# Kernel optimization log

Hardware: AMD Instinct MI355X
Metric: run time of the kernel (lower is better)

## Reference

```python
import jax, jax.numpy as jnp
import numpy as np

HEAD_SIZE = 64   # baseChn * max_channel_ratio
NUM_HEADS = 2
LEAKY_ALPHA = 0.3  # tf.keras.layers.LeakyReLU default


def setup_inputs() -> dict:
    key = jax.random.key(0)
    ks = jax.random.split(key, 6)
    x = jax.random.normal(ks[0], (96, 48, 512), dtype=jnp.float32)
    y = jax.random.uniform(ks[1], (96, 64, 64), dtype=jnp.float32)
    nItem = jax.random.uniform(ks[2], (96,), dtype=jnp.float32, minval=1.0, maxval=48.0)
    W_proj = jax.random.normal(ks[3], (512, 64), dtype=jnp.float32) * 0.05
    W1 = jax.random.normal(ks[4], (64, 128), dtype=jnp.float32) * 0.1
    W2 = jax.random.normal(ks[5], (2, 1), dtype=jnp.float32)
    return {"x": x, "y": y, "nItem": nItem, "W_proj": W_proj, "W1": W1, "W2": W2}


def reference(x, y, nItem, W_proj, W1, W2):
    # fc_cnn_proj: Dense(64, gelu exact, no bias)
    gallery = jax.nn.gelu(jnp.matmul(x, W_proj), approximate=False)  # [Sx, Nx, 64]
    Sx, Nx, _ = gallery.shape
    Sy, Ny, _ = y.shape
    sqrt_hs = jnp.sqrt(jnp.float32(HEAD_SIZE))
    # shared linear (no bias) then split heads: [S, H, N, hs]
    px = jnp.matmul(gallery, W1).reshape(Sx, Nx, NUM_HEADS, HEAD_SIZE).transpose(0, 2, 1, 3)
    py = jnp.matmul(y, W1).reshape(Sy, Ny, NUM_HEADS, HEAD_SIZE).transpose(0, 2, 1, 3)
    # pairwise cross-set attention maps: [Sy, Sx, H, Ny, Nx]
    att = jnp.einsum('yhmd,xhnd->yxhmn', py, px) / sqrt_hs
    att = jnp.where(att > 0, att, LEAKY_ALPHA * att)
    # reduce over both item axes, normalize by nItem[x] and nItemMax_y
    sc = att.sum(axis=(3, 4)) / nItem[None, :, None] / jnp.float32(Ny)  # [Sy, Sx, H]
    scores = jnp.matmul(sc, W2)  # linear2: Dense(1, no bias) -> [Sy, Sx, 1]
    return scores
```

## Files before the change

kernel.cpp:

```cpp
#include <hip/hip_runtime.h>
#include <hip/hip_bf16.h>


typedef short bf16x8 __attribute__((ext_vector_type(8)));
typedef float f32x4 __attribute__((ext_vector_type(4)));

__device__ __forceinline__ unsigned short f2bf(float v) {
  __hip_bfloat16 b = __float2bfloat16(v);
  return *reinterpret_cast<unsigned short*>(&b);
}

__device__ __forceinline__ bf16x8 load8_cvt(const float* __restrict__ p) {
  f32x4 v0 = *reinterpret_cast<const f32x4*>(p);
  f32x4 v1 = *reinterpret_cast<const f32x4*>(p + 4);
  bf16x8 r;
  r[0] = (short)f2bf(v0[0]); r[1] = (short)f2bf(v0[1]);
  r[2] = (short)f2bf(v0[2]); r[3] = (short)f2bf(v0[3]);
  r[4] = (short)f2bf(v1[0]); r[5] = (short)f2bf(v1[1]);
  r[6] = (short)f2bf(v1[2]); r[7] = (short)f2bf(v1[3]);
  return r;
}

__global__ __launch_bounds__(256) void k_prep(const float* __restrict__ x,
                                              const float* __restrict__ y,
                                              const float* __restrict__ Wp,
                                              const float* __restrict__ W1,
                                              unsigned short* __restrict__ pyf,
                                              unsigned short* __restrict__ pxf) {
  __shared__ unsigned short w1f[8192];
  __shared__ unsigned short wpf[8192];
  __shared__ unsigned short gal[4][1152];
  int t = threadIdx.x;
  int lane = t & 63, w = t >> 6;
  int b = blockIdx.x;

#pragma unroll
  for (int it = 0; it < 32; ++it) {
    int idx = it * 256 + t;
    int k = idx >> 7, d = idx & 127;
    int l = (d & 15) + 16 * ((k >> 3) & 3);
    int f = (k >> 5) * 8 + (d >> 4);
    w1f[f * 512 + l * 8 + (k & 7)] = f2bf(W1[idx]);
  }
  if (b >= 72) {
    __syncthreads();
    int yi = b - 72;
    const bf16x8* WF = reinterpret_cast<const bf16x8*>(w1f);
    int row0 = yi * 64 + w * 16 + (lane & 15);
    const float* yb = y + (size_t)row0 * 64 + 8 * (lane >> 4);
    bf16x8 a0 = load8_cvt(yb);
    bf16x8 a1 = load8_cvt(yb + 32);
    f32x4 acc[8];
#pragma unroll
    for (int nt = 0; nt < 8; ++nt) acc[nt] = (f32x4){0.f, 0.f, 0.f, 0.f};
#pragma unroll
    for (int nt = 0; nt < 8; ++nt) {
      acc[nt] = __builtin_amdgcn_mfma_f32_16x16x32_bf16(a0, WF[nt * 64 + lane], acc[nt], 0, 0, 0);
      acc[nt] = __builtin_amdgcn_mfma_f32_16x16x32_bf16(a1, WF[(8 + nt) * 64 + lane], acc[nt], 0, 0, 0);
    }
    int r_hi = (lane >> 4) * 4;
#pragma unroll
    for (int nt = 0; nt < 8; ++nt) {
      int d = nt * 16 + (lane & 15);
      int h = d >> 6, dd = d & 63;
      int kc = dd >> 5, q = (dd >> 3) & 3, i = dd & 7;
#pragma unroll
      for (int j = 0; j < 4; ++j) {
        int m = w * 16 + r_hi + j;
        int mt = m >> 4, rr = m & 15;
        size_t idx = ((size_t)((yi * 2 + h) * 8 + mt * 2 + kc)) * 512 + (rr + (q << 4)) * 8 + i;
        pyf[idx] = f2bf(acc[nt][j]);
      }
    }
  } else {
    int rowbase = b * 64;
    const bf16x8* WPF = reinterpret_cast<const bf16x8*>(wpf);
    const bf16x8* WF = reinterpret_cast<const bf16x8*>(w1f);
    int rloc = rowbase + w * 16 + (lane & 15);
    const float* xb = x + (size_t)rloc * 512 + 8 * (lane >> 4);
    f32x4 acc1[4];
#pragma unroll
    for (int nt = 0; nt < 4; ++nt) acc1[nt] = (f32x4){0.f, 0.f, 0.f, 0.f};
#pragma unroll
    for (int q = 0; q < 4; ++q) {
      if (q) __syncthreads();
#pragma unroll
      for (int it = 0; it < 32; ++it) {
        int idx = it * 256 + t;
        int kq = idx >> 6, c = idx & 63;
        int l = (c & 15) + 16 * ((kq >> 3) & 3);
        int g = ((kq >> 5) & 3) * 4 + (c >> 4);
        wpf[g * 512 + l * 8 + (kq & 7)] = f2bf(Wp[(q * 128 + kq) * 64 + c]);
      }
      __syncthreads();
#pragma unroll
      for (int kk = 0; kk < 4; ++kk) {
        int kc = q * 4 + kk;
        bf16x8 a = load8_cvt(xb + 32 * kc);
#pragma unroll
        for (int nt = 0; nt < 4; ++nt)
          acc1[nt] = __builtin_amdgcn_mfma_f32_16x16x32_bf16(a, WPF[(kk * 4 + nt) * 64 + lane], acc1[nt], 0, 0, 0);
      }
    }
#pragma unroll
    for (int nt = 0; nt < 4; ++nt)
#pragma unroll
      for (int j = 0; j < 4; ++j) {
        float s = acc1[nt][j];
        float ge = 0.5f * s * (1.0f + erff(s * 0.70710678118654752f));
        int rl = (lane >> 4) * 4 + j;
        int c = nt * 16 + (lane & 15);
        gal[w][rl * 72 + c] = f2bf(ge);
      }
    const unsigned short* gp = &gal[w][(lane & 15) * 72 + 8 * (lane >> 4)];
    bf16x8 g0 = *reinterpret_cast<const bf16x8*>(gp);
    bf16x8 g1 = *reinterpret_cast<const bf16x8*>(gp + 32);
    f32x4 acc2[8];
#pragma unroll
    for (int nt = 0; nt < 8; ++nt) acc2[nt] = (f32x4){0.f, 0.f, 0.f, 0.f};
#pragma unroll
    for (int nt = 0; nt < 8; ++nt) {
      acc2[nt] = __builtin_amdgcn_mfma_f32_16x16x32_bf16(g0, WF[nt * 64 + lane], acc2[nt], 0, 0, 0);
      acc2[nt] = __builtin_amdgcn_mfma_f32_16x16x32_bf16(g1, WF[(8 + nt) * 64 + lane], acc2[nt], 0, 0, 0);
    }
    int r_hi = (lane >> 4) * 4;
#pragma unroll
    for (int nt = 0; nt < 8; ++nt) {
      int d = nt * 16 + (lane & 15);
      int h = d >> 6, dd = d & 63;
      int kc = dd >> 5, q2 = (dd >> 3) & 3, i = dd & 7;
#pragma unroll
      for (int j = 0; j < 4; ++j) {
        int row = rowbase + w * 16 + r_hi + j;
        int xi = row / 48, n = row % 48;
        int nt3 = n >> 4, rr = n & 15;
        size_t idx = ((size_t)((xi * 2 + h) * 6 + nt3 * 2 + kc)) * 512 + (rr + (q2 << 4)) * 8 + i;
        pxf[idx] = f2bf(acc2[nt][j]);
      }
    }
  }
}

__global__ __launch_bounds__(256) void k_att(const unsigned short* __restrict__ pyf_u,
                                             const unsigned short* __restrict__ pxf_u,
                                             const float* __restrict__ nItem,
                                             const float* __restrict__ W2,
                                             float* __restrict__ out) {
  int lane = threadIdx.x & 63;
  int w = threadIdx.x >> 6;
  int bid = blockIdx.x;
  int yb = bid >> 5, xq = bid & 31;
  int yi = yb * 4 + w;
  int xi0 = xq * 3;
  const bf16x8* PA = reinterpret_cast<const bf16x8*>(pyf_u);
  const bf16x8* PB = reinterpret_cast<const bf16x8*>(pxf_u);

  float w2h0 = W2[0], w2h1 = W2[1];
  float nI0 = nItem[xi0], nI1 = nItem[xi0 + 1], nI2 = nItem[xi0 + 2];

  f32x4 zero4 = {0.f, 0.f, 0.f, 0.f};
  asm volatile("" : "+v"(zero4));

  bf16x8 A8[16];
  size_t abase = (size_t)(yi * 2) * 512 + lane;
#pragma unroll
  for (int f = 0; f < 8; ++f) {
    A8[f]     = PA[abase + f * 64];
    A8[8 + f] = PA[abase + 512 + f * 64];
  }

  float c3h0 = 0.3f * w2h0, c7h0 = 0.7f * w2h0;
  float c3h1 = 0.3f * w2h1, c7h1 = 0.7f * w2h1;

  bf16x8 Bc[6], Bn[6];
  size_t bb0 = (size_t)((xi0 * 2 + 0) * 6) * 64 + lane;
#pragma unroll
  for (int f = 0; f < 6; ++f) Bc[f] = PB[bb0 + f * 64];

  f32x4 res4[3];
#pragma unroll
  for (int g = 0; g < 3; ++g) res4[g] = (f32x4){0.f, 0.f, 0.f, 0.f};

#pragma unroll
  for (int s = 0; s < 6; ++s) {
    const int h = s / 3, g = s % 3;
    if (s < 5) {
      const int s2 = s + 1, h2 = s2 / 3, g2 = s2 % 3;
      size_t bb = (size_t)(((xi0 + g2) * 2 + h2) * 6) * 64 + lane;
#pragma unroll
      for (int f = 0; f < 6; ++f) Bn[f] = PB[bb + f * 64];
    }
    const float c3 = h ? c3h1 : c3h0;
    const float c7 = h ? c7h1 : c7h0;
#pragma unroll
    for (int nt = 0; nt < 3; ++nt)
#pragma unroll
      for (int mt = 0; mt < 4; ++mt) {
        f32x4 acc = __builtin_amdgcn_mfma_f32_16x16x32_bf16(A8[h * 8 + mt * 2], Bc[nt * 2], zero4, 0, 0, 0);
        acc = __builtin_amdgcn_mfma_f32_16x16x32_bf16(A8[h * 8 + mt * 2 + 1], Bc[nt * 2 + 1], acc, 0, 0, 0);
        f32x4 mx = {fmaxf(acc[0], 0.f), fmaxf(acc[1], 0.f), fmaxf(acc[2], 0.f), fmaxf(acc[3], 0.f)};
        res4[g] += acc * c3;
        res4[g] += mx * c7;
      }
#pragma unroll
    for (int f = 0; f < 6; ++f) Bc[f] = Bn[f];
  }

  float tot0 = (res4[0][0] + res4[0][1]) + (res4[0][2] + res4[0][3]);
  float tot1 = (res4[1][0] + res4[1][1]) + (res4[1][2] + res4[1][3]);
  float tot2 = (res4[2][0] + res4[2][1]) + (res4[2][2] + res4[2][3]);
#pragma unroll
  for (int off = 32; off >= 1; off >>= 1) {
    tot0 += __shfl_xor(tot0, off, 64);
    tot1 += __shfl_xor(tot1, off, 64);
    tot2 += __shfl_xor(tot2, off, 64);
  }
  if (lane == 0) {
    out[yi * 96 + xi0 + 0] = tot0 / (512.0f * nI0);
    out[yi * 96 + xi0 + 1] = tot1 / (512.0f * nI1);
    out[yi * 96 + xi0 + 2] = tot2 / (512.0f * nI2);
  }
}

extern "C" void kernel_launch(void* const* d_in, const int* in_sizes, int n_in,
                              void* d_out, int out_size, void* d_ws, size_t ws_size,
                              hipStream_t stream) {
  const float* x     = (const float*)d_in[0];
  const float* y     = (const float*)d_in[1];
  const float* nItem = (const float*)d_in[2];
  const float* Wp    = (const float*)d_in[3];
  const float* W1    = (const float*)d_in[4];
  const float* W2    = (const float*)d_in[5];
  float* out = (float*)d_out;

  unsigned short* pyf = (unsigned short*)d_ws;
  unsigned short* pxf = pyf + 786432;

  hipLaunchKernelGGL(k_prep, dim3(168), dim3(256), 0, stream, x, y, Wp, W1, pyf, pxf);
  hipLaunchKernelGGL(k_att, dim3(768), dim3(256), 0, stream, pyf, pxf, nItem, W2, out);
}
```

Before: 35.52 us.

## Fuse prep and attention kernels with a device-wide atomic barrier

Merges the projection kernel and the attention kernel into one persistent launch of 384 blocks. The first 168 blocks compute the projections, then every block waits on a grid-wide barrier built from atomic counters, with one leader block per XCD issuing a release before all blocks proceed. Each block then handles six x-items instead of three, halving the attention grid. This removes a kernel launch boundary and its tail, but adds a memset launch and spin-waiting, and it relies on all 384 blocks being co-resident to avoid deadlock.

```diff
diff --git a/kernel.cpp b/kernel.cpp
--- a/kernel.cpp
+++ b/kernel.cpp
@@ -4,6 +4,12 @@
 
 typedef short bf16x8 __attribute__((ext_vector_type(8)));
 typedef float f32x4 __attribute__((ext_vector_type(4)));
+
+#define NPROD 168u
+#define NBLK  384
+#define F_PRODCNT 0
+#define F_FLUSHCNT 1
+#define F_CLAIM 2
 
 __device__ __forceinline__ unsigned short f2bf(float v) {
   __hip_bfloat16 b = __float2bfloat16(v);
@@ -21,12 +27,16 @@
   return r;
 }
 
-__global__ __launch_bounds__(256) void k_prep(const float* __restrict__ x,
-                                              const float* __restrict__ y,
-                                              const float* __restrict__ Wp,
-                                              const float* __restrict__ W1,
-                                              unsigned short* __restrict__ pyf,
-                                              unsigned short* __restrict__ pxf) {
+__global__ __launch_bounds__(256, 2) void k_fused(const float* __restrict__ x,
+                                                  const float* __restrict__ y,
+                                                  const float* __restrict__ Wp,
+                                                  const float* __restrict__ W1,
+                                                  const float* __restrict__ nItem,
+                                                  const float* __restrict__ W2,
+                                                  unsigned short* __restrict__ pyf,
+                                                  unsigned short* __restrict__ pxf,
+                                                  unsigned int* flags,
+                                                  float* __restrict__ out) {
   __shared__ unsigned short w1f[8192];
   __shared__ unsigned short wpf[8192];
   __shared__ unsigned short gal[4][1152];
@@ -34,191 +44,202 @@
   int lane = t & 63, w = t >> 6;
   int b = blockIdx.x;
 
-#pragma unroll
-  for (int it = 0; it < 32; ++it) {
-    int idx = it * 256 + t;
-    int k = idx >> 7, d = idx & 127;
-    int l = (d & 15) + 16 * ((k >> 3) & 3);
-    int f = (k >> 5) * 8 + (d >> 4);
-    w1f[f * 512 + l * 8 + (k & 7)] = f2bf(W1[idx]);
+  float w2h0 = W2[0], w2h1 = W2[1];
+  int xi0 = (b & 15) * 6;
+  float nI[6];
+#pragma unroll
+  for (int g = 0; g < 6; ++g) nI[g] = nItem[xi0 + g];
+
+  if (b < (int)NPROD) {
+#pragma unroll
+    for (int it = 0; it < 32; ++it) {
+      int idx = it * 256 + t;
+      int k = idx >> 7, d = idx & 127;
+      int l = (d & 15) + 16 * ((k >> 3) & 3);
+      int f = (k >> 5) * 8 + (d >> 4);
+      w1f[f * 512 + l * 8 + (k & 7)] = f2bf(W1[idx]);
+    }
+    if (b >= 72) {
+      __syncthreads();
+      int yi = b - 72;
+      const bf16x8* WF = reinterpret_cast<const bf16x8*>(w1f);
+      int row0 = yi * 64 + w * 16 + (lane & 15);
+      const float* yb = y + (size_t)row0 * 64 + 8 * (lane >> 4);
+      bf16x8 a0 = load8_cvt(yb);
+      bf16x8 a1 = load8_cvt(yb + 32);
+      f32x4 acc[8];
+#pragma unroll
+      for (int nt = 0; nt < 8; ++nt) acc[nt] = (f32x4){0.f, 0.f, 0.f, 0.f};
+#pragma unroll
+      for (int nt = 0; nt < 8; ++nt) {
+        acc[nt] = __builtin_amdgcn_mfma_f32_16x16x32_bf16(a0, WF[nt * 64 + lane], acc[nt], 0, 0, 0);
+        acc[nt] = __builtin_amdgcn_mfma_f32_16x16x32_bf16(a1, WF[(8 + nt) * 64 + lane], acc[nt], 0, 0, 0);
+      }
+      int r_hi = (lane >> 4) * 4;
+#pragma unroll
+      for (int nt = 0; nt < 8; ++nt) {
+        int d = nt * 16 + (lane & 15);
+        int h = d >> 6, dd = d & 63;
+        int kc = dd >> 5, q = (dd >> 3) & 3, i = dd & 7;
+#pragma unroll
+        for (int j = 0; j < 4; ++j) {
+          int m = w * 16 + r_hi + j;
+          int mt = m >> 4, rr = m & 15;
+          size_t idx = ((size_t)((yi * 2 + h) * 8 + mt * 2 + kc)) * 512 + (rr + (q << 4)) * 8 + i;
+          pyf[idx] = f2bf(acc[nt][j]);
+        }
+      }
+    } else {
+      int rowbase = b * 64;
+      const bf16x8* WPF = reinterpret_cast<const bf16x8*>(wpf);
+      const bf16x8* WF = reinterpret_cast<const bf16x8*>(w1f);
+      int rloc = rowbase + w * 16 + (lane & 15);
+      const float* xb = x + (size_t)rloc * 512 + 8 * (lane >> 4);
+      f32x4 acc1[4];
+#pragma unroll
+      for (int nt = 0; nt < 4; ++nt) acc1[nt] = (f32x4){0.f, 0.f, 0.f, 0.f};
+#pragma unroll
+      for (int q = 0; q < 4; ++q) {
+        if (q) __syncthreads();
+#pragma unroll
+        for (int it = 0; it < 32; ++it) {
+          int idx = it * 256 + t;
+          int kq = idx >> 6, c = idx & 63;
+          int l = (c & 15) + 16 * ((kq >> 3) & 3);
+          int g = ((kq >> 5) & 3) * 4 + (c >> 4);
+          wpf[g * 512 + l * 8 + (kq & 7)] = f2bf(Wp[(q * 128 + kq) * 64 + c]);
+        }
+        __syncthreads();
+#pragma unroll
+        for (int kk = 0; kk < 4; ++kk) {
+          int kc = q * 4 + kk;
+          bf16x8 a = load8_cvt(xb + 32 * kc);
+#pragma unroll
+          for (int nt = 0; nt < 4; ++nt)
+            acc1[nt] = __builtin_amdgcn_mfma_f32_16x16x32_bf16(a, WPF[(kk * 4 + nt) * 64 + lane], acc1[nt], 0, 0, 0);
+        }
+      }
+#pragma unroll
+      for (int nt = 0; nt < 4; ++nt)
+#pragma unroll
+        for (int j = 0; j < 4; ++j) {
+          float s = acc1[nt][j];
+          float ge = 0.5f * s * (1.0f + erff(s * 0.70710678118654752f));
+          int rl = (lane >> 4) * 4 + j;
+          int c = nt * 16 + (lane & 15);
+          gal[w][rl * 72 + c] = f2bf(ge);
+        }
+      const unsigned short* gp = &gal[w][(lane & 15) * 72 + 8 * (lane >> 4)];
+      bf16x8 g0 = *reinterpret_cast<const bf16x8*>(gp);
+      bf16x8 g1 = *reinterpret_cast<const bf16x8*>(gp + 32);
+      f32x4 acc2[8];
+#pragma unroll
+      for (int nt = 0; nt < 8; ++nt) acc2[nt] = (f32x4){0.f, 0.f, 0.f, 0.f};
+#pragma unroll
+      for (int nt = 0; nt < 8; ++nt) {
+        acc2[nt] = __builtin_amdgcn_mfma_f32_16x16x32_bf16(g0, WF[nt * 64 + lane], acc2[nt], 0, 0, 0);
+        acc2[nt] = __builtin_amdgcn_mfma_f32_16x16x32_bf16(g1, WF[(8 + nt) * 64 + lane], acc2[nt], 0, 0, 0);
+      }
+      int r_hi = (lane >> 4) * 4;
+#pragma unroll
+      for (int nt = 0; nt < 8; ++nt) {
+        int d = nt * 16 + (lane & 15);
+        int h = d >> 6, dd = d & 63;
+        int kc = dd >> 5, q2 = (dd >> 3) & 3, i = dd & 7;
+#pragma unroll
+        for (int j = 0; j < 4; ++j) {
+          int row = rowbase + w * 16 + r_hi + j;
+          int xi = row / 48, n = row % 48;
+          int nt3 = n >> 4, rr = n & 15;
+          size_t idx = ((size_t)((xi * 2 + h) * 6 + nt3 * 2 + kc)) * 512 + (rr + (q2 << 4)) * 8 + i;
+          pxf[idx] = f2bf(acc2[nt][j]);
+        }
+      }
+    }
   }
-  if (b >= 72) {
-    __syncthreads();
-    int yi = b - 72;
-    const bf16x8* WF = reinterpret_cast<const bf16x8*>(w1f);
-    int row0 = yi * 64 + w * 16 + (lane & 15);
-    const float* yb = y + (size_t)row0 * 64 + 8 * (lane >> 4);
-    bf16x8 a0 = load8_cvt(yb);
-    bf16x8 a1 = load8_cvt(yb + 32);
-    f32x4 acc[8];
-#pragma unroll
-    for (int nt = 0; nt < 8; ++nt) acc[nt] = (f32x4){0.f, 0.f, 0.f, 0.f};
-#pragma unroll
-    for (int nt = 0; nt < 8; ++nt) {
-      acc[nt] = __builtin_amdgcn_mfma_f32_16x16x32_bf16(a0, WF[nt * 64 + lane], acc[nt], 0, 0, 0);
-      acc[nt] = __builtin_amdgcn_mfma_f32_16x16x32_bf16(a1, WF[(8 + nt) * 64 + lane], acc[nt], 0, 0, 0);
-    }
-    int r_hi = (lane >> 4) * 4;
-#pragma unroll
-    for (int nt = 0; nt < 8; ++nt) {
-      int d = nt * 16 + (lane & 15);
-      int h = d >> 6, dd = d & 63;
-      int kc = dd >> 5, q = (dd >> 3) & 3, i = dd & 7;
-#pragma unroll
-      for (int j = 0; j < 4; ++j) {
-        int m = w * 16 + r_hi + j;
-        int mt = m >> 4, rr = m & 15;
-        size_t idx = ((size_t)((yi * 2 + h) * 8 + mt * 2 + kc)) * 512 + (rr + (q << 4)) * 8 + i;
-        pyf[idx] = f2bf(acc[nt][j]);
-      }
-    }
-  } else {
-    int rowbase = b * 64;
-    const bf16x8* WPF = reinterpret_cast<const bf16x8*>(wpf);
-    const bf16x8* WF = reinterpret_cast<const bf16x8*>(w1f);
-    int rloc = rowbase + w * 16 + (lane & 15);
-    const float* xb = x + (size_t)rloc * 512 + 8 * (lane >> 4);
-    f32x4 acc1[4];
-#pragma unroll
-    for (int nt = 0; nt < 4; ++nt) acc1[nt] = (f32x4){0.f, 0.f, 0.f, 0.f};
-#pragma unroll
-    for (int q = 0; q < 4; ++q) {
-      if (q) __syncthreads();
-#pragma unroll
-      for (int it = 0; it < 32; ++it) {
-        int idx = it * 256 + t;
-        int kq = idx >> 6, c = idx & 63;
-        int l = (c & 15) + 16 * ((kq >> 3) & 3);
-        int g = ((kq >> 5) & 3) * 4 + (c >> 4);
-        wpf[g * 512 + l * 8 + (kq & 7)] = f2bf(Wp[(q * 128 + kq) * 64 + c]);
-      }
-      __syncthreads();
-#pragma unroll
-      for (int kk = 0; kk < 4; ++kk) {
-        int kc = q * 4 + kk;
-        bf16x8 a = load8_cvt(xb + 32 * kc);
-#pragma unroll
-        for (int nt = 0; nt < 4; ++nt)
-          acc1[nt] = __builtin_amdgcn_mfma_f32_16x16x32_bf16(a, WPF[(kk * 4 + nt) * 64 + lane], acc1[nt], 0, 0, 0);
-      }
-    }
-#pragma unroll
-    for (int nt = 0; nt < 4; ++nt)
-#pragma unroll
-      for (int j = 0; j < 4; ++j) {
-        float s = acc1[nt][j];
-        float ge = 0.5f * s * (1.0f + erff(s * 0.70710678118654752f));
-        int rl = (lane >> 4) * 4 + j;
-        int c = nt * 16 + (lane & 15);
-        gal[w][rl * 72 + c] = f2bf(ge);
-      }
-    const unsigned short* gp = &gal[w][(lane & 15) * 72 + 8 * (lane >> 4)];
-    bf16x8 g0 = *reinterpret_cast<const bf16x8*>(gp);
-    bf16x8 g1 = *reinterpret_cast<const bf16x8*>(gp + 32);
-    f32x4 acc2[8];
-#pragma unroll
-    for (int nt = 0; nt < 8; ++nt) acc2[nt] = (f32x4){0.f, 0.f, 0.f, 0.f};
-#pragma unroll
-    for (int nt = 0; nt < 8; ++nt) {
-      acc2[nt] = __builtin_amdgcn_mfma_f32_16x16x32_bf16(g0, WF[nt * 64 + lane], acc2[nt], 0, 0, 0);
-      acc2[nt] = __builtin_amdgcn_mfma_f32_16x16x32_bf16(g1, WF[(8 + nt) * 64 + lane], acc2[nt], 0, 0, 0);
-    }
-    int r_hi = (lane >> 4) * 4;
-#pragma unroll
-    for (int nt = 0; nt < 8; ++nt) {
-      int d = nt * 16 + (lane & 15);
-      int h = d >> 6, dd = d & 63;
-      int kc = dd >> 5, q2 = (dd >> 3) & 3, i = dd & 7;
-#pragma unroll
-      for (int j = 0; j < 4; ++j) {
-        int row = rowbase + w * 16 + r_hi + j;
-        int xi = row / 48, n = row % 48;
-        int nt3 = n >> 4, rr = n & 15;
-        size_t idx = ((size_t)((xi * 2 + h) * 6 + nt3 * 2 + kc)) * 512 + (rr + (q2 << 4)) * 8 + i;
-        pxf[idx] = f2bf(acc2[nt][j]);
-      }
-    }
+
+  __syncthreads();
+  if (t == 0) {
+    if (b < (int)NPROD)
+      __hip_atomic_fetch_add(&flags[F_PRODCNT], 1u, __ATOMIC_RELAXED, __HIP_MEMORY_SCOPE_AGENT);
+    unsigned xcd;
+    asm volatile("s_getreg_b32 %0, hwreg(HW_REG_XCC_ID)" : "=s"(xcd));
+    xcd &= 7u;
+    if (__hip_atomic_fetch_add(&flags[F_CLAIM + xcd], 1u, __ATOMIC_RELAXED, __HIP_MEMORY_SCOPE_AGENT) == 0u) {
+      while (__hip_atomic_load(&flags[F_PRODCNT], __ATOMIC_RELAXED, __HIP_MEMORY_SCOPE_AGENT) != NPROD)
+        __builtin_amdgcn_s_sleep(4);
+      __hip_atomic_fetch_add(&flags[F_FLUSHCNT], 1u, __ATOMIC_RELEASE, __HIP_MEMORY_SCOPE_AGENT);
+    }
+    while (__hip_atomic_load(&flags[F_FLUSHCNT], __ATOMIC_RELAXED, __HIP_MEMORY_SCOPE_AGENT) != 8u)
+      __builtin_amdgcn_s_sleep(4);
   }
-}
-
-__global__ __launch_bounds__(256) void k_att(const unsigned short* __restrict__ pyf_u,
-                                             const unsigned short* __restrict__ pxf_u,
-                                             const float* __restrict__ nItem,
-                                             const float* __restrict__ W2,
-                                             float* __restrict__ out) {
-  int lane = threadIdx.x & 63;
-  int w = threadIdx.x >> 6;
-  int bid = blockIdx.x;
-  int yb = bid >> 5, xq = bid & 31;
-  int yi = yb * 4 + w;
-  int xi0 = xq * 3;
-  const bf16x8* PA = reinterpret_cast<const bf16x8*>(pyf_u);
-  const bf16x8* PB = reinterpret_cast<const bf16x8*>(pxf_u);
-
-  float w2h0 = W2[0], w2h1 = W2[1];
-  float nI0 = nItem[xi0], nI1 = nItem[xi0 + 1], nI2 = nItem[xi0 + 2];
-
-  f32x4 zero4 = {0.f, 0.f, 0.f, 0.f};
-  asm volatile("" : "+v"(zero4));
-
-  bf16x8 A8[16];
-  size_t abase = (size_t)(yi * 2) * 512 + lane;
-#pragma unroll
-  for (int f = 0; f < 8; ++f) {
-    A8[f]     = PA[abase + f * 64];
-    A8[8 + f] = PA[abase + 512 + f * 64];
-  }
-
-  float c3h0 = 0.3f * w2h0, c7h0 = 0.7f * w2h0;
-  float c3h1 = 0.3f * w2h1, c7h1 = 0.7f * w2h1;
-
-  bf16x8 Bc[6], Bn[6];
-  size_t bb0 = (size_t)((xi0 * 2 + 0) * 6) * 64 + lane;
-#pragma unroll
-  for (int f = 0; f < 6; ++f) Bc[f] = PB[bb0 + f * 64];
-
-  f32x4 res4[3];
-#pragma unroll
-  for (int g = 0; g < 3; ++g) res4[g] = (f32x4){0.f, 0.f, 0.f, 0.f};
-
-#pragma unroll
-  for (int s = 0; s < 6; ++s) {
-    const int h = s / 3, g = s % 3;
-    if (s < 5) {
-      const int s2 = s + 1, h2 = s2 / 3, g2 = s2 % 3;
-      size_t bb = (size_t)(((xi0 + g2) * 2 + h2) * 6) * 64 + lane;
-#pragma unroll
-      for (int f = 0; f < 6; ++f) Bn[f] = PB[bb + f * 64];
-    }
-    const float c3 = h ? c3h1 : c3h0;
-    const float c7 = h ? c7h1 : c7h0;
-#pragma unroll
-    for (int nt = 0; nt < 3; ++nt)
-#pragma unroll
-      for (int mt = 0; mt < 4; ++mt) {
-        f32x4 acc = __builtin_amdgcn_mfma_f32_16x16x32_bf16(A8[h * 8 + mt * 2], Bc[nt * 2], zero4, 0, 0, 0);
-        acc = __builtin_amdgcn_mfma_f32_16x16x32_bf16(A8[h * 8 + mt * 2 + 1], Bc[nt * 2 + 1], acc, 0, 0, 0);
-        f32x4 mx = {fmaxf(acc[0], 0.f), fmaxf(acc[1], 0.f), fmaxf(acc[2], 0.f), fmaxf(acc[3], 0.f)};
-        res4[g] += acc * c3;
-        res4[g] += mx * c7;
-      }
-#pragma unroll
-    for (int f = 0; f < 6; ++f) Bc[f] = Bn[f];
-  }
-
-  float tot0 = (res4[0][0] + res4[0][1]) + (res4[0][2] + res4[0][3]);
-  float tot1 = (res4[1][0] + res4[1][1]) + (res4[1][2] + res4[1][3]);
-  float tot2 = (res4[2][0] + res4[2][1]) + (res4[2][2] + res4[2][3]);
-#pragma unroll
-  for (int off = 32; off >= 1; off >>= 1) {
-    tot0 += __shfl_xor(tot0, off, 64);
-    tot1 += __shfl_xor(tot1, off, 64);
-    tot2 += __shfl_xor(tot2, off, 64);
-  }
-  if (lane == 0) {
-    out[yi * 96 + xi0 + 0] = tot0 / (512.0f * nI0);
-    out[yi * 96 + xi0 + 1] = tot1 / (512.0f * nI1);
-    out[yi * 96 + xi0 + 2] = tot2 / (512.0f * nI2);
+  __syncthreads();
+
+  {
+    int yi = (b >> 4) * 4 + w;
+    const bf16x8* PA = reinterpret_cast<const bf16x8*>(pyf);
+    const bf16x8* PB = reinterpret_cast<const bf16x8*>(pxf);
+
+    f32x4 zero4 = {0.f, 0.f, 0.f, 0.f};
+    asm volatile("" : "+v"(zero4));
+
+    bf16x8 A8[16];
+    size_t abase = (size_t)(yi * 2) * 512 + lane;
+#pragma unroll
+    for (int f = 0; f < 8; ++f) {
+      A8[f]     = PA[abase + f * 64];
+      A8[8 + f] = PA[abase + 512 + f * 64];
+    }
+    float c3h0 = 0.3f * w2h0, c7h0 = 0.7f * w2h0;
+    float c3h1 = 0.3f * w2h1, c7h1 = 0.7f * w2h1;
+
+    bf16x8 Bc[6], Bn[6];
+    size_t bb0 = (size_t)((xi0 * 2 + 0) * 6) * 64 + lane;
+#pragma unroll
+    for (int f = 0; f < 6; ++f) Bc[f] = PB[bb0 + f * 64];
+
+    f32x4 res4[6];
+#pragma unroll
+    for (int g = 0; g < 6; ++g) res4[g] = (f32x4){0.f, 0.f, 0.f, 0.f};
+
+#pragma unroll
+    for (int s = 0; s < 12; ++s) {
+      const int h = s & 1, g = s >> 1;
+      if (s < 11) {
+        const int s2 = s + 1, h2 = s2 & 1, g2 = s2 >> 1;
+        size_t bb = (size_t)(((xi0 + g2) * 2 + h2) * 6) * 64 + lane;
+#pragma unroll
+        for (int f = 0; f < 6; ++f) Bn[f] = PB[bb + f * 64];
+      }
+      const float c3 = h ? c3h1 : c3h0;
+      const float c7 = h ? c7h1 : c7h0;
+#pragma unroll
+      for (int nt = 0; nt < 3; ++nt)
+#pragma unroll
+        for (int mt = 0; mt < 4; ++mt) {
+          f32x4 acc = __builtin_amdgcn_mfma_f32_16x16x32_bf16(A8[h * 8 + mt * 2], Bc[nt * 2], zero4, 0, 0, 0);
+          acc = __builtin_amdgcn_mfma_f32_16x16x32_bf16(A8[h * 8 + mt * 2 + 1], Bc[nt * 2 + 1], acc, 0, 0, 0);
+          f32x4 mx = {fmaxf(acc[0], 0.f), fmaxf(acc[1], 0.f), fmaxf(acc[2], 0.f), fmaxf(acc[3], 0.f)};
+          res4[g] += acc * c3;
+          res4[g] += mx * c7;
+        }
+#pragma unroll
+      for (int f = 0; f < 6; ++f) Bc[f] = Bn[f];
+    }
+
+    float tot[6];
+#pragma unroll
+    for (int g = 0; g < 6; ++g)
+      tot[g] = (res4[g][0] + res4[g][1]) + (res4[g][2] + res4[g][3]);
+#pragma unroll
+    for (int off = 32; off >= 1; off >>= 1)
+#pragma unroll
+      for (int g = 0; g < 6; ++g) tot[g] += __shfl_xor(tot[g], off, 64);
+    if (lane == 0) {
+#pragma unroll
+      for (int g = 0; g < 6; ++g)
+        out[yi * 96 + xi0 + g] = tot[g] / (512.0f * nI[g]);
+    }
   }
 }
 
@@ -235,7 +256,9 @@
 
   unsigned short* pyf = (unsigned short*)d_ws;
   unsigned short* pxf = pyf + 786432;
-
-  hipLaunchKernelGGL(k_prep, dim3(168), dim3(256), 0, stream, x, y, Wp, W1, pyf, pxf);
-  hipLaunchKernelGGL(k_att, dim3(768), dim3(256), 0, stream, pyf, pxf, nItem, W2, out);
-}
+  unsigned int* flags = (unsigned int*)(pxf + 589824);
+
+  hipMemsetAsync(flags, 0, 64, stream);
+  hipLaunchKernelGGL(k_fused, dim3(NBLK), dim3(256), 0, stream,
+                     x, y, Wp, W1, nItem, W2, pyf, pxf, flags, out);
+}
```

Result: slower. 55.16 us (+55.3%).

## Pre-swizzle weights to bf16 in a separate kernel and double prep block count

Applied to the files above, without the earlier changes.

A new small kernel converts Wp and W1 to bf16 in MFMA fragment layout once. The prep kernel then copies these layouts into LDS with vector loads instead of having every block convert them element by element. Each prep block now handles 32 rows instead of 64, doubling the grid from 168 to 336 blocks, with the four waves splitting the N tiles. The aim is more parallelism and less redundant weight conversion per block, at the cost of an extra kernel launch and more repeated weight loads in total.

```diff
diff --git a/kernel.cpp b/kernel.cpp
--- a/kernel.cpp
+++ b/kernel.cpp
@@ -21,121 +21,122 @@
   return r;
 }
 
-__global__ __launch_bounds__(256) void k_prep(const float* __restrict__ x,
-                                              const float* __restrict__ y,
-                                              const float* __restrict__ Wp,
-                                              const float* __restrict__ W1,
-                                              unsigned short* __restrict__ pyf,
-                                              unsigned short* __restrict__ pxf) {
+__global__ __launch_bounds__(256) void k_wprep(const float* __restrict__ Wp,
+                                               const float* __restrict__ W1,
+                                               unsigned short* __restrict__ WpF,
+                                               unsigned short* __restrict__ W1F) {
+  int tid = blockIdx.x * 256 + threadIdx.x;
+  if (tid < 32768) {
+    int kc = tid >> 11, nt = (tid >> 9) & 3, l = (tid >> 3) & 63, i = tid & 7;
+    int k = 32 * kc + 8 * (l >> 4) + i, c = nt * 16 + (l & 15);
+    WpF[tid] = f2bf(Wp[k * 64 + c]);
+  } else {
+    int t2 = tid - 32768;
+    int kc = t2 >> 12, nt = (t2 >> 9) & 7, l = (t2 >> 3) & 63, i = t2 & 7;
+    int k = 32 * kc + 8 * (l >> 4) + i, d = nt * 16 + (l & 15);
+    W1F[t2] = f2bf(W1[k * 128 + d]);
+  }
+}
+
+__global__ __launch_bounds__(256, 3) void k_prep2(const float* __restrict__ x,
+                                                  const float* __restrict__ y,
+                                                  const unsigned short* __restrict__ WpF_u,
+                                                  const unsigned short* __restrict__ W1F_u,
+                                                  unsigned short* __restrict__ pyf,
+                                                  unsigned short* __restrict__ pxf) {
   __shared__ unsigned short w1f[8192];
-  __shared__ unsigned short wpf[8192];
-  __shared__ unsigned short gal[4][1152];
+  __shared__ unsigned short wpq[16384];
+  __shared__ unsigned short gal[32 * 72];
   int t = threadIdx.x;
   int lane = t & 63, w = t >> 6;
   int b = blockIdx.x;
 
-#pragma unroll
-  for (int it = 0; it < 32; ++it) {
-    int idx = it * 256 + t;
-    int k = idx >> 7, d = idx & 127;
-    int l = (d & 15) + 16 * ((k >> 3) & 3);
-    int f = (k >> 5) * 8 + (d >> 4);
-    w1f[f * 512 + l * 8 + (k & 7)] = f2bf(W1[idx]);
-  }
-  if (b >= 72) {
+  const bf16x8* W1Fg = reinterpret_cast<const bf16x8*>(W1F_u);
+  const bf16x8* WPFg = reinterpret_cast<const bf16x8*>(WpF_u);
+  const bf16x8* WF = reinterpret_cast<const bf16x8*>(w1f);
+  const bf16x8* WPQ = reinterpret_cast<const bf16x8*>(wpq);
+
+#pragma unroll
+  for (int it = 0; it < 4; ++it)
+    reinterpret_cast<bf16x8*>(w1f)[it * 256 + t] = W1Fg[it * 256 + t];
+
+  f32x4 zero4 = {0.f, 0.f, 0.f, 0.f};
+  asm volatile("" : "+v"(zero4));
+
+  if (b < 144) {
+    int rowbase = b * 32;
+    int rt = w & 1, ntp = (w >> 1) * 2;
+    const float* xa = x + (size_t)(rowbase + rt * 16 + (lane & 15)) * 512 + 8 * (lane >> 4);
+    f32x4 acc[2] = {{0, 0, 0, 0}, {0, 0, 0, 0}};
+#pragma unroll
+    for (int hf = 0; hf < 2; ++hf) {
+      if (hf) __syncthreads();
+#pragma unroll
+      for (int it = 0; it < 8; ++it)
+        reinterpret_cast<bf16x8*>(wpq)[it * 256 + t] = WPFg[hf * 2048 + it * 256 + t];
+      __syncthreads();
+#pragma unroll
+      for (int kcl = 0; kcl < 8; ++kcl) {
+        bf16x8 a = load8_cvt(xa + 32 * (hf * 8 + kcl));
+#pragma unroll
+        for (int u = 0; u < 2; ++u)
+          acc[u] = __builtin_amdgcn_mfma_f32_16x16x32_bf16(a, WPQ[(kcl * 4 + ntp + u) * 64 + lane], acc[u], 0, 0, 0);
+      }
+    }
+#pragma unroll
+    for (int u = 0; u < 2; ++u)
+#pragma unroll
+      for (int j = 0; j < 4; ++j) {
+        float s = acc[u][j];
+        float ge = 0.5f * s * (1.0f + erff(s * 0.70710678118654752f));
+        int lr = rt * 16 + (lane >> 4) * 4 + j;
+        int c = (ntp + u) * 16 + (lane & 15);
+        gal[lr * 72 + c] = f2bf(ge);
+      }
     __syncthreads();
-    int yi = b - 72;
-    const bf16x8* WF = reinterpret_cast<const bf16x8*>(w1f);
-    int row0 = yi * 64 + w * 16 + (lane & 15);
-    const float* yb = y + (size_t)row0 * 64 + 8 * (lane >> 4);
-    bf16x8 a0 = load8_cvt(yb);
-    bf16x8 a1 = load8_cvt(yb + 32);
-    f32x4 acc[8];
-#pragma unroll
-    for (int nt = 0; nt < 8; ++nt) acc[nt] = (f32x4){0.f, 0.f, 0.f, 0.f};
-#pragma unroll
-    for (int nt = 0; nt < 8; ++nt) {
-      acc[nt] = __builtin_amdgcn_mfma_f32_16x16x32_bf16(a0, WF[nt * 64 + lane], acc[nt], 0, 0, 0);
-      acc[nt] = __builtin_amdgcn_mfma_f32_16x16x32_bf16(a1, WF[(8 + nt) * 64 + lane], acc[nt], 0, 0, 0);
-    }
-    int r_hi = (lane >> 4) * 4;
-#pragma unroll
-    for (int nt = 0; nt < 8; ++nt) {
-      int d = nt * 16 + (lane & 15);
-      int h = d >> 6, dd = d & 63;
-      int kc = dd >> 5, q = (dd >> 3) & 3, i = dd & 7;
-#pragma unroll
-      for (int j = 0; j < 4; ++j) {
-        int m = w * 16 + r_hi + j;
-        int mt = m >> 4, rr = m & 15;
-        size_t idx = ((size_t)((yi * 2 + h) * 8 + mt * 2 + kc)) * 512 + (rr + (q << 4)) * 8 + i;
-        pyf[idx] = f2bf(acc[nt][j]);
-      }
-    }
-  } else {
-    int rowbase = b * 64;
-    const bf16x8* WPF = reinterpret_cast<const bf16x8*>(wpf);
-    const bf16x8* WF = reinterpret_cast<const bf16x8*>(w1f);
-    int rloc = rowbase + w * 16 + (lane & 15);
-    const float* xb = x + (size_t)rloc * 512 + 8 * (lane >> 4);
-    f32x4 acc1[4];
-#pragma unroll
-    for (int nt = 0; nt < 4; ++nt) acc1[nt] = (f32x4){0.f, 0.f, 0.f, 0.f};
-#pragma unroll
-    for (int q = 0; q < 4; ++q) {
-      if (q) __syncthreads();
-#pragma unroll
-      for (int it = 0; it < 32; ++it) {
-        int idx = it * 256 + t;
-        int kq = idx >> 6, c = idx & 63;
-        int l = (c & 15) + 16 * ((kq >> 3) & 3);
-        int g = ((kq >> 5) & 3) * 4 + (c >> 4);
-        wpf[g * 512 + l * 8 + (kq & 7)] = f2bf(Wp[(q * 128 + kq) * 64 + c]);
-      }
-      __syncthreads();
-#pragma unroll
-      for (int kk = 0; kk < 4; ++kk) {
-        int kc = q * 4 + kk;
-        bf16x8 a = load8_cvt(xb + 32 * kc);
-#pragma unroll
-        for (int nt = 0; nt < 4; ++nt)
-          acc1[nt] = __builtin_amdgcn_mfma_f32_16x16x32_bf16(a, WPF[(kk * 4 + nt) * 64 + lane], acc1[nt], 0, 0, 0);
-      }
-    }
-#pragma unroll
-    for (int nt = 0; nt < 4; ++nt)
-#pragma unroll
-      for (int j = 0; j < 4; ++j) {
-        float s = acc1[nt][j];
-        float ge = 0.5f * s * (1.0f + erff(s * 0.70710678118654752f));
-        int rl = (lane >> 4) * 4 + j;
-        int c = nt * 16 + (lane & 15);
-        gal[w][rl * 72 + c] = f2bf(ge);
-      }
-    const unsigned short* gp = &gal[w][(lane & 15) * 72 + 8 * (lane >> 4)];
+    int nb = (w >> 1) * 4;
+    const unsigned short* gp = &gal[(rt * 16 + (lane & 15)) * 72 + 8 * (lane >> 4)];
     bf16x8 g0 = *reinterpret_cast<const bf16x8*>(gp);
     bf16x8 g1 = *reinterpret_cast<const bf16x8*>(gp + 32);
-    f32x4 acc2[8];
-#pragma unroll
-    for (int nt = 0; nt < 8; ++nt) acc2[nt] = (f32x4){0.f, 0.f, 0.f, 0.f};
-#pragma unroll
-    for (int nt = 0; nt < 8; ++nt) {
-      acc2[nt] = __builtin_amdgcn_mfma_f32_16x16x32_bf16(g0, WF[nt * 64 + lane], acc2[nt], 0, 0, 0);
-      acc2[nt] = __builtin_amdgcn_mfma_f32_16x16x32_bf16(g1, WF[(8 + nt) * 64 + lane], acc2[nt], 0, 0, 0);
-    }
-    int r_hi = (lane >> 4) * 4;
-#pragma unroll
-    for (int nt = 0; nt < 8; ++nt) {
-      int d = nt * 16 + (lane & 15);
+#pragma unroll
+    for (int v = 0; v < 4; ++v) {
+      int nt2 = nb + v;
+      f32x4 acc2 = __builtin_amdgcn_mfma_f32_16x16x32_bf16(g0, WF[nt2 * 64 + lane], zero4, 0, 0, 0);
+      acc2 = __builtin_amdgcn_mfma_f32_16x16x32_bf16(g1, WF[(8 + nt2) * 64 + lane], acc2, 0, 0, 0);
+      int d = nt2 * 16 + (lane & 15);
       int h = d >> 6, dd = d & 63;
       int kc = dd >> 5, q2 = (dd >> 3) & 3, i = dd & 7;
 #pragma unroll
       for (int j = 0; j < 4; ++j) {
-        int row = rowbase + w * 16 + r_hi + j;
+        int row = rowbase + rt * 16 + (lane >> 4) * 4 + j;
         int xi = row / 48, n = row % 48;
         int nt3 = n >> 4, rr = n & 15;
         size_t idx = ((size_t)((xi * 2 + h) * 6 + nt3 * 2 + kc)) * 512 + (rr + (q2 << 4)) * 8 + i;
-        pxf[idx] = f2bf(acc2[nt][j]);
+        pxf[idx] = f2bf(acc2[j]);
+      }
+    }
+  } else {
+    __syncthreads();
+    int b2 = b - 144;
+    int mt = w & 1, nb = (w >> 1) * 4;
+    const float* ybp = y + (size_t)(b2 * 32 + mt * 16 + (lane & 15)) * 64 + 8 * (lane >> 4);
+    bf16x8 a0 = load8_cvt(ybp);
+    bf16x8 a1 = load8_cvt(ybp + 32);
+#pragma unroll
+    for (int v = 0; v < 4; ++v) {
+      int nt2 = nb + v;
+      f32x4 acc = __builtin_amdgcn_mfma_f32_16x16x32_bf16(a0, WF[nt2 * 64 + lane], zero4, 0, 0, 0);
+      acc = __builtin_amdgcn_mfma_f32_16x16x32_bf16(a1, WF[(8 + nt2) * 64 + lane], acc, 0, 0, 0);
+      int d = nt2 * 16 + (lane & 15);
+      int h = d >> 6, dd = d & 63;
+      int kc = dd >> 5, q2 = (dd >> 3) & 3, i = dd & 7;
+#pragma unroll
+      for (int j = 0; j < 4; ++j) {
+        int row = b2 * 32 + mt * 16 + (lane >> 4) * 4 + j;
+        int yi = row >> 6, m = row & 63;
+        int mt3 = m >> 4, rr = m & 15;
+        size_t idx = ((size_t)((yi * 2 + h) * 8 + mt3 * 2 + kc)) * 512 + (rr + (q2 << 4)) * 8 + i;
+        pyf[idx] = f2bf(acc[j]);
       }
     }
   }
@@ -168,7 +169,6 @@
     A8[f]     = PA[abase + f * 64];
     A8[8 + f] = PA[abase + 512 + f * 64];
   }
-
   float c3h0 = 0.3f * w2h0, c7h0 = 0.7f * w2h0;
   float c3h1 = 0.3f * w2h1, c7h1 = 0.7f * w2h1;
 
@@ -233,9 +233,12 @@
   const float* W2    = (const float*)d_in[5];
   float* out = (float*)d_out;
 
-  unsigned short* pyf = (unsigned short*)d_ws;
+  unsigned short* WpF = (unsigned short*)d_ws;
+  unsigned short* W1F = WpF + 32768;
+  unsigned short* pyf = W1F + 8192;
   unsigned short* pxf = pyf + 786432;
 
-  hipLaunchKernelGGL(k_prep, dim3(168), dim3(256), 0, stream, x, y, Wp, W1, pyf, pxf);
+  hipLaunchKernelGGL(k_wprep, dim3(160), dim3(256), 0, stream, Wp, W1, WpF, W1F);
+  hipLaunchKernelGGL(k_prep2, dim3(336), dim3(256), 0, stream, x, y, WpF, W1F, pyf, pxf);
   hipLaunchKernelGGL(k_att, dim3(768), dim3(256), 0, stream, pyf, pxf, nItem, W2, out);
 }
```

After: 38.64 us. +8.8%, slower.
